# Kernel optimization log

Measured on AMD Instinct MI355X. Metric: run time of the kernel, lower is better.

The kernel has to match this reference:

```python
import jax, jax.numpy as jnp
import numpy as np

HX_INIT = 1e-6  # matches torch: zeros + 1e-06


def log_g(x):
    # log of continuous activation g: x>=0 -> log(x+0.5), else log(sigmoid(x)) = -softplus(-x)
    return jnp.where(x >= 0, jnp.log(jax.nn.relu(x) + 0.5), -jax.nn.softplus(-x))


def setup_inputs() -> dict:
    key = jax.random.key(0)
    k1, k2, k3 = jax.random.split(key, 3)
    N, L, H_in, H = 8, 4096, 512, 512
    x = jax.random.normal(k1, (N, L, H_in), dtype=jnp.float32)
    W = jax.random.normal(k2, (3 * H, H_in), dtype=jnp.float32) * 0.05
    b = jax.random.normal(k3, (3 * H,), dtype=jnp.float32) * 0.05
    return {"x": x, "W": W, "b": b}


def reference(x, W, b):
    N, L, _ = x.shape
    H = W.shape[0] // 3
    # gate preactivations: (N, L, 3H)
    pre = jnp.einsum('nli,oi->nlo', x, W) + b
    f_pre, i_pre, h_pre = jnp.split(pre, 3, axis=-1)
    # log-space gates
    diff = jax.nn.softplus(-f_pre) - jax.nn.softplus(-i_pre)
    log_f = -jax.nn.softplus(diff)       # log f'_t
    log_i = -jax.nn.softplus(-diff)      # log i'_t
    log_tilde_h = log_g(h_pre)
    # initial hidden state hx = 1e-6 (zeros + eps), shape (N, 1, H)
    log_h0 = jnp.full((N, 1, H), jnp.log(jnp.asarray(HX_INIT, x.dtype)), dtype=x.dtype)
    log_values = jnp.concatenate([log_h0, log_i + log_tilde_h], axis=1)  # (N, L+1, H)
    # Heinsen log-space parallel scan
    a_star = jnp.pad(jnp.cumsum(log_f, axis=1), ((0, 0), (1, 0), (0, 0)))  # (N, L+1, H)
    log_h = a_star + jax.lax.cumlogsumexp(log_values - a_star, axis=1)
    return jnp.exp(log_h)[:, 1:]  # (N, L, H)
```

## Files before the change

### kernel.cpp

```cpp
#include <hip/hip_runtime.h>
#include <hip/hip_bf16.h>


#define H_DIM 512
#define LSEQ 4096
#define NBATCH 8
#define M_TOTAL (NBATCH * LSEQ)

#define BM 128
#define BK 64

#define CS 128
#define NC 32

typedef __attribute__((ext_vector_type(8))) short short8;
typedef __attribute__((ext_vector_type(4))) float floatx4;
typedef __attribute__((ext_vector_type(4))) float float4v;
typedef _Float16 h2 __attribute__((ext_vector_type(2)));
typedef _Float16 h8 __attribute__((ext_vector_type(8)));
typedef __attribute__((ext_vector_type(2))) float float2v;
typedef __attribute__((ext_vector_type(2))) unsigned int uint2v;

#define NEG_BIG (-1.0e30f)
#define C_LOG2E 1.4426950408889634f
#define LOG2_HX0 (-19.931568569324174f)

__device__ __forceinline__ float exp2_hw(float x) {
#if __has_builtin(__builtin_amdgcn_exp2f)
    return __builtin_amdgcn_exp2f(x);
#else
    return exp2f(x);
#endif
}

__device__ __forceinline__ float log2_hw(float x) {
#if __has_builtin(__builtin_amdgcn_logf)
    return __builtin_amdgcn_logf(x);
#else
    return log2f(x);
#endif
}

__device__ __forceinline__ float logaddexp2_f(float p, float q) {
    float m = fmaxf(p, q);
    float d = -fabsf(p - q);
    return m + log2_hw(1.0f + exp2_hw(d));
}

__device__ __forceinline__ float bf16u_to_f(unsigned short u) {
    unsigned int w = ((unsigned int)u) << 16;
    float f;
    __builtin_memcpy(&f, &w, 4);
    return f;
}

__device__ __forceinline__ unsigned short f_to_bf16u(float f) {
    __hip_bfloat16 h = __float2bfloat16(f);
    unsigned short u;
    __builtin_memcpy(&u, &h, 2);
    return u;
}

__device__ __forceinline__ void gload_lds16(const void* g, void* l) {
    __builtin_amdgcn_global_load_lds(
        (const __attribute__((address_space(1))) unsigned int*)g,
        (__attribute__((address_space(3))) unsigned int*)l, 16, 0, 0);
}

__global__ void detect_and_bias(const unsigned short* __restrict__ xu,
                                const void* __restrict__ bsrc,
                                int* __restrict__ flag,
                                float* __restrict__ bdst) {
    __shared__ int cnt;
    if (threadIdx.x == 0) cnt = 0;
    __syncthreads();
    const short8* x8 = (const short8*)xu;
    int local = 0;
    #pragma unroll
    for (int j = 0; j < 8; j++) {
        short8 v = x8[threadIdx.x + j * 256];
        #pragma unroll
        for (int e = 0; e < 8; e++) {
            unsigned short u = (unsigned short)v[e];
            if (((u >> 7) & 0xFF) == 0xFF) local++;
        }
    }
    if (local) atomicAdd(&cnt, local);
    __syncthreads();
    int f = (cnt > 8) ? 1 : 0;
    if (threadIdx.x == 0) flag[0] = f;
    #pragma unroll
    for (int j = 0; j < 6; j++) {
        int i = threadIdx.x + j * 256;
        bdst[i] = f ? ((const float*)bsrc)[i]
                    : bf16u_to_f(((const unsigned short*)bsrc)[i]);
    }
}

__global__ __launch_bounds__(256)
void convert_inputs(const void* __restrict__ x, const void* __restrict__ W,
                    unsigned short* __restrict__ xc,
                    unsigned short* __restrict__ Wc,
                    const int* __restrict__ flag) {
    const int bx = blockIdx.x;
    const void* src;
    unsigned short* dst;
    int i;
    if (bx < 8192) { src = x; dst = xc; i = (bx * 256 + threadIdx.x) * 8; }
    else           { src = W; dst = Wc; i = ((bx - 8192) * 256 + threadIdx.x) * 8; }
    if (*flag) {
        const float4v* s4 = (const float4v*)((const float*)src + i);
        float4v a = s4[0], b = s4[1];
        short8 v;
        v[0] = (short)f_to_bf16u(a[0]); v[1] = (short)f_to_bf16u(a[1]);
        v[2] = (short)f_to_bf16u(a[2]); v[3] = (short)f_to_bf16u(a[3]);
        v[4] = (short)f_to_bf16u(b[0]); v[5] = (short)f_to_bf16u(b[1]);
        v[6] = (short)f_to_bf16u(b[2]); v[7] = (short)f_to_bf16u(b[3]);
        *(short8*)&dst[i] = v;
    } else {
        *(short8*)&dst[i] = *(const short8*)&((const short*)src)[i];
    }
}

__global__ __launch_bounds__(256, 3)
void gemm_gates(const unsigned short* __restrict__ x,
                const unsigned short* __restrict__ W,
                const float* __restrict__ bias,
                h2* __restrict__ plv,
                float* __restrict__ Asum, float* __restrict__ Bval,
                float* __restrict__ Asub, float* __restrict__ Bsub) {
    __shared__ __align__(16) char ldsbuf[40960];
    short* Alds = (short*)ldsbuf;
    short* Blds = (short*)(ldsbuf + 16384);
    h2* sc = (h2*)ldsbuf;
    float* sa = (float*)(ldsbuf + 32768);
    float* sb = sa + 256;

    const int by = blockIdx.x;
    const int bx = blockIdx.y;
    const int tid = threadIdx.x;
    const int lane = tid & 63;
    const int w = tid >> 6;
    const int wr = (w >> 1) * 64;
    const int wc2 = w & 1;
    const int l8 = lane >> 3, s8 = lane & 7;
    const int sg = s8 ^ l8;
    const int fr = lane & 15;
    const int q = lane >> 4;

    const int R0 = by * BM;

    floatx4 acc[4][6];
    #pragma unroll
    for (int i = 0; i < 4; i++)
        #pragma unroll
        for (int j = 0; j < 6; j++)
            acc[i][j] = (floatx4){0.f, 0.f, 0.f, 0.f};

    const short* xg = (const short*)x;
    const short* wg = (const short*)W;

    for (int k0 = 0; k0 < H_DIM; k0 += BK) {
        __syncthreads();
        #pragma unroll
        for (int i = 0; i < 4; i++) {
            int c = w * 4 + i;
            const short* g = xg + (size_t)(R0 + c * 8 + l8) * H_DIM + k0 + sg * 8;
            gload_lds16(g, &Alds[c * 512]);
        }
        #pragma unroll
        for (int i = 0; i < 6; i++) {
            int c = w * 6 + i;
            int br = c * 8 + l8;
            int wrow = (br >> 6) * H_DIM + bx * 64 + (br & 63);
            const short* g = wg + (size_t)wrow * H_DIM + k0 + sg * 8;
            gload_lds16(g, &Blds[c * 512]);
        }
        __syncthreads();

        #pragma unroll
        for (int ks = 0; ks < 2; ks++) {
            const int s = ks * 4 + q;
            short8 af[4], bf[6];
            #pragma unroll
            for (int mt = 0; mt < 4; mt++) {
                int ar = wr + mt * 16 + fr;
                af[mt] = *(const short8*)&Alds[ar * BK + ((s ^ (ar & 7)) << 3)];
            }
            #pragma unroll
            for (int j = 0; j < 6; j++) {
                int nt = (j >> 1) * 4 + wc2 * 2 + (j & 1);
                int brr = nt * 16 + fr;
                bf[j] = *(const short8*)&Blds[brr * BK + ((s ^ (brr & 7)) << 3)];
            }
            #pragma unroll
            for (int mt = 0; mt < 4; mt++)
                #pragma unroll
                for (int j = 0; j < 6; j++)
                    acc[mt][j] = __builtin_amdgcn_mfma_f32_16x16x32_bf16(
                        af[mt], bf[j], acc[mt][j], 0, 0, 0);
        }
    }

    __syncthreads();

    const int rowb = R0 + wr + q * 4;
    const int tloc0 = wr + q * 4;
    #pragma unroll
    for (int jj = 0; jj < 2; jj++) {
        int hl = wc2 * 32 + jj * 16 + fr;
        int hcol = bx * 64 + hl;
        float bfv = bias[hcol];
        float biv = bias[H_DIM + hcol];
        float bhv = bias[2 * H_DIM + hcol];
        float bf2 = -bfv * C_LOG2E;
        float bi2 = -biv * C_LOG2E;
        #pragma unroll
        for (int mt = 0; mt < 4; mt++) {
            #pragma unroll
            for (int r = 0; r < 4; r++) {
                float ef = exp2_hw(fminf(fmaf(acc[mt][jj][r], -C_LOG2E, bf2), 126.0f));
                float ei = exp2_hw(fminf(fmaf(acc[mt][2 + jj][r], -C_LOG2E, bi2), 126.0f));
                float hp = acc[mt][4 + jj][r] + bhv;
                float eh = exp2_hw(fminf(-hp * C_LOG2E, 126.0f));
                float afv = 1.0f + ef, aiv = 1.0f + ei;
                float sfi = afv + aiv;
                float ls = log2_hw(sfi);
                float lf = log2_hw(aiv) - ls;
                float marg = (hp >= 0.0f) ? (hp + 0.5f) : (1.0f + eh);
                float lm = log2_hw(marg);
                float lg = (hp >= 0.0f) ? lm : -lm;
                float lv = (log2_hw(afv) - ls) + lg;
                int row = rowb + mt * 16 + r;
                h2 pk;
                pk[0] = (_Float16)lf;
                pk[1] = (_Float16)lv;
                plv[(size_t)row * H_DIM + hcol] = pk;
                sc[(tloc0 + mt * 16 + r) * 64 + hl] = pk;
            }
        }
    }

    __syncthreads();

    const int n = by >> 5, c = by & 31;
    {
        float a = 0.f, bacc = NEG_BIG;
        const int t0 = w * 32;
        #pragma unroll 4
        for (int t = t0; t < t0 + 32; t++) {
            h2 p = sc[t * 64 + lane];
            float f = (float)p[0];
            bacc = logaddexp2_f(f + bacc, (float)p[1]);
            a += f;
        }
        sa[w * 64 + lane] = a;
        sb[w * 64 + lane] = bacc;
        size_t o = (((size_t)n * NC + c) * 4 + w) * H_DIM + bx * 64 + lane;
        Asub[o] = a;
        Bsub[o] = bacc;
    }
    __syncthreads();

    if (w == 0) {
        float a = sa[lane], b = sb[lane];
        #pragma unroll
        for (int s = 1; s < 4; s++) {
            float as = sa[s * 64 + lane], bs = sb[s * 64 + lane];
            b = logaddexp2_f(as + b, bs);
            a += as;
        }
        size_t o = ((size_t)n * NC + c) * H_DIM + bx * 64 + lane;
        Asum[o] = a;
        Bval[o] = b;
    }
}

__global__ __launch_bounds__(256)
void scan_apply(const h2* __restrict__ plv,
                const float* __restrict__ Asum, const float* __restrict__ Bval,
                const float* __restrict__ Asub, const float* __restrict__ Bsub,
                void* __restrict__ outv, const int* __restrict__ flag) {
    const int cc = blockIdx.x;
    const int n = blockIdx.y;
    const int c = cc & 31;
    const int s = (cc >> 5) * 2 + (threadIdx.x >> 7);
    const int h0 = (threadIdx.x & 127) * 4;
    const int f32out = *flag;

    float r0 = LOG2_HX0, r1 = r0, r2 = r0, r3 = r0;
    size_t so = (size_t)n * NC * H_DIM + h0;
    int cp = 0;
    for (; cp + 4 <= c; cp += 4) {
        float4v A0 = *(const float4v*)&Asum[so + (size_t)(cp + 0) * H_DIM];
        float4v B0 = *(const float4v*)&Bval[so + (size_t)(cp + 0) * H_DIM];
        float4v A1 = *(const float4v*)&Asum[so + (size_t)(cp + 1) * H_DIM];
        float4v B1 = *(const float4v*)&Bval[so + (size_t)(cp + 1) * H_DIM];
        float4v A2 = *(const float4v*)&Asum[so + (size_t)(cp + 2) * H_DIM];
        float4v B2 = *(const float4v*)&Bval[so + (size_t)(cp + 2) * H_DIM];
        float4v A3 = *(const float4v*)&Asum[so + (size_t)(cp + 3) * H_DIM];
        float4v B3 = *(const float4v*)&Bval[so + (size_t)(cp + 3) * H_DIM];
        r0 = logaddexp2_f(A0[0] + r0, B0[0]); r1 = logaddexp2_f(A0[1] + r1, B0[1]);
        r2 = logaddexp2_f(A0[2] + r2, B0[2]); r3 = logaddexp2_f(A0[3] + r3, B0[3]);
        r0 = logaddexp2_f(A1[0] + r0, B1[0]); r1 = logaddexp2_f(A1[1] + r1, B1[1]);
        r2 = logaddexp2_f(A1[2] + r2, B1[2]); r3 = logaddexp2_f(A1[3] + r3, B1[3]);
        r0 = logaddexp2_f(A2[0] + r0, B2[0]); r1 = logaddexp2_f(A2[1] + r1, B2[1]);
        r2 = logaddexp2_f(A2[2] + r2, B2[2]); r3 = logaddexp2_f(A2[3] + r3, B2[3]);
        r0 = logaddexp2_f(A3[0] + r0, B3[0]); r1 = logaddexp2_f(A3[1] + r1, B3[1]);
        r2 = logaddexp2_f(A3[2] + r2, B3[2]); r3 = logaddexp2_f(A3[3] + r3, B3[3]);
    }
    for (; cp < c; cp++) {
        float4v A = *(const float4v*)&Asum[so + (size_t)cp * H_DIM];
        float4v B = *(const float4v*)&Bval[so + (size_t)cp * H_DIM];
        r0 = logaddexp2_f(A[0] + r0, B[0]); r1 = logaddexp2_f(A[1] + r1, B[1]);
        r2 = logaddexp2_f(A[2] + r2, B[2]); r3 = logaddexp2_f(A[3] + r3, B[3]);
    }
    size_t sub = (((size_t)n * NC + c) * 4) * H_DIM + h0;
    for (int sp = 0; sp < s; sp++) {
        float4v A = *(const float4v*)&Asub[sub + (size_t)sp * H_DIM];
        float4v B = *(const float4v*)&Bsub[sub + (size_t)sp * H_DIM];
        r0 = logaddexp2_f(A[0] + r0, B[0]); r1 = logaddexp2_f(A[1] + r1, B[1]);
        r2 = logaddexp2_f(A[2] + r2, B[2]); r3 = logaddexp2_f(A[3] + r3, B[3]);
    }

    size_t base = ((size_t)n * LSEQ + (size_t)c * CS + s * 32) * H_DIM + h0;
    if (f32out) {
        float* of = (float*)outv;
        #pragma unroll 4
        for (int t = 0; t < 32; t++) {
            size_t idx = base + (size_t)t * H_DIM;
            h8 p = *(const h8*)&plv[idx];
            r0 = logaddexp2_f((float)p[0] + r0, (float)p[1]);
            r1 = logaddexp2_f((float)p[2] + r1, (float)p[3]);
            r2 = logaddexp2_f((float)p[4] + r2, (float)p[5]);
            r3 = logaddexp2_f((float)p[6] + r3, (float)p[7]);
            float4v o4 = {exp2_hw(r0), exp2_hw(r1), exp2_hw(r2), exp2_hw(r3)};
            *(float4v*)&of[idx] = o4;
        }
    } else {
        unsigned int* ob32 = (unsigned int*)outv;
        #pragma unroll 4
        for (int t = 0; t < 32; t++) {
            size_t idx = base + (size_t)t * H_DIM;
            h8 p = *(const h8*)&plv[idx];
            r0 = logaddexp2_f((float)p[0] + r0, (float)p[1]);
            r1 = logaddexp2_f((float)p[2] + r1, (float)p[3]);
            r2 = logaddexp2_f((float)p[4] + r2, (float)p[5]);
            r3 = logaddexp2_f((float)p[6] + r3, (float)p[7]);
            uint2v pk;
            pk[0] = ((unsigned int)f_to_bf16u(exp2_hw(r1)) << 16) | f_to_bf16u(exp2_hw(r0));
            pk[1] = ((unsigned int)f_to_bf16u(exp2_hw(r3)) << 16) | f_to_bf16u(exp2_hw(r2));
            *(uint2v*)&ob32[idx >> 1] = pk;
        }
    }
}

extern "C" void kernel_launch(void* const* d_in, const int* in_sizes, int n_in,
                              void* d_out, int out_size, void* d_ws, size_t ws_size,
                              hipStream_t stream) {
    const void* x = d_in[0];
    const void* W = d_in[1];
    const void* b = d_in[2];

    char* wsb = (char*)d_ws;
    int* flag            = (int*)wsb;
    float* bconv         = (float*)(wsb + 16);
    unsigned short* xc   = (unsigned short*)(wsb + 16384);
    unsigned short* Wc   = (unsigned short*)(wsb + 16384 + 33554432);
    h2* plv              = (h2*)(wsb + 36700160);
    float* Asum          = (float*)(wsb + 103809024);
    float* Bval          = (float*)(wsb + 104333312);
    float* Asub          = (float*)(wsb + 104857600);
    float* Bsub          = (float*)(wsb + 106954752);

    detect_and_bias<<<1, 256, 0, stream>>>((const unsigned short*)x, b, flag, bconv);
    convert_inputs<<<8576, 256, 0, stream>>>(x, W, xc, Wc, flag);

    dim3 g1(M_TOTAL / BM, H_DIM / 64);
    gemm_gates<<<g1, 256, 0, stream>>>(xc, Wc, bconv, plv, Asum, Bval, Asub, Bsub);

    dim3 g2(NC * 2, NBATCH);
    scan_apply<<<g2, 256, 0, stream>>>(plv, Asum, Bval, Asub, Bsub, d_out, flag);
}
```

Baseline: 212.4 us.

## Fuse scan into GEMM kernel via decoupled look-back across sequence chunks

```diff
diff --git a/kernel.cpp b/kernel.cpp
--- a/kernel.cpp
+++ b/kernel.cpp
@@ -17,9 +17,6 @@
 typedef __attribute__((ext_vector_type(4))) float floatx4;
 typedef __attribute__((ext_vector_type(4))) float float4v;
 typedef _Float16 h2 __attribute__((ext_vector_type(2)));
-typedef _Float16 h8 __attribute__((ext_vector_type(8)));
-typedef __attribute__((ext_vector_type(2))) float float2v;
-typedef __attribute__((ext_vector_type(2))) unsigned int uint2v;
 
 #define NEG_BIG (-1.0e30f)
 #define C_LOG2E 1.4426950408889634f
@@ -126,15 +123,17 @@
 void gemm_gates(const unsigned short* __restrict__ x,
                 const unsigned short* __restrict__ W,
                 const float* __restrict__ bias,
-                h2* __restrict__ plv,
-                float* __restrict__ Asum, float* __restrict__ Bval,
-                float* __restrict__ Asub, float* __restrict__ Bsub) {
+                float* __restrict__ aggA, float* __restrict__ aggB,
+                float* __restrict__ incA, float* __restrict__ incB,
+                int* __restrict__ flags,
+                void* __restrict__ outv, const int* __restrict__ oflag) {
     __shared__ __align__(16) char ldsbuf[40960];
     short* Alds = (short*)ldsbuf;
     short* Blds = (short*)(ldsbuf + 16384);
     h2* sc = (h2*)ldsbuf;
     float* sa = (float*)(ldsbuf + 32768);
-    float* sb = sa + 256;
+    float* sb = (float*)(ldsbuf + 33792);
+    float* carr = (float*)(ldsbuf + 34816);
 
     const int by = blockIdx.x;
     const int bx = blockIdx.y;
@@ -204,7 +203,6 @@
 
     __syncthreads();
 
-    const int rowb = R0 + wr + q * 4;
     const int tloc0 = wr + q * 4;
     #pragma unroll
     for (int jj = 0; jj < 2; jj++) {
@@ -231,11 +229,9 @@
                 float lm = log2_hw(marg);
                 float lg = (hp >= 0.0f) ? lm : -lm;
                 float lv = (log2_hw(afv) - ls) + lg;
-                int row = rowb + mt * 16 + r;
                 h2 pk;
                 pk[0] = (_Float16)lf;
                 pk[1] = (_Float16)lv;
-                plv[(size_t)row * H_DIM + hcol] = pk;
                 sc[(tloc0 + mt * 16 + r) * 64 + hl] = pk;
             }
         }
@@ -243,7 +239,8 @@
 
     __syncthreads();
 
-    const int n = by >> 5, c = by & 31;
+    const int c = by & 31;
+    const int fidx = by * 8 + bx;
     {
         float a = 0.f, bacc = NEG_BIG;
         const int t0 = w * 32;
@@ -256,101 +253,92 @@
         }
         sa[w * 64 + lane] = a;
         sb[w * 64 + lane] = bacc;
-        size_t o = (((size_t)n * NC + c) * 4 + w) * H_DIM + bx * 64 + lane;
-        Asub[o] = a;
-        Bsub[o] = bacc;
     }
     __syncthreads();
 
     if (w == 0) {
-        float a = sa[lane], b = sb[lane];
+        float Ac = sa[lane], Bc = sb[lane];
         #pragma unroll
         for (int s = 1; s < 4; s++) {
             float as = sa[s * 64 + lane], bs = sb[s * 64 + lane];
-            b = logaddexp2_f(as + b, bs);
-            a += as;
-        }
-        size_t o = ((size_t)n * NC + c) * H_DIM + bx * 64 + lane;
-        Asum[o] = a;
-        Bval[o] = b;
-    }
-}
-
-__global__ __launch_bounds__(256)
-void scan_apply(const h2* __restrict__ plv,
-                const float* __restrict__ Asum, const float* __restrict__ Bval,
-                const float* __restrict__ Asub, const float* __restrict__ Bsub,
-                void* __restrict__ outv, const int* __restrict__ flag) {
-    const int cc = blockIdx.x;
-    const int n = blockIdx.y;
-    const int c = cc & 31;
-    const int s = (cc >> 5) * 2 + (threadIdx.x >> 7);
-    const int h0 = (threadIdx.x & 127) * 4;
-    const int f32out = *flag;
-
-    float r0 = LOG2_HX0, r1 = r0, r2 = r0, r3 = r0;
-    size_t so = (size_t)n * NC * H_DIM + h0;
-    int cp = 0;
-    for (; cp + 4 <= c; cp += 4) {
-        float4v A0 = *(const float4v*)&Asum[so + (size_t)(cp + 0) * H_DIM];
-        float4v B0 = *(const float4v*)&Bval[so + (size_t)(cp + 0) * H_DIM];
-        float4v A1 = *(const float4v*)&Asum[so + (size_t)(cp + 1) * H_DIM];
-        float4v B1 = *(const float4v*)&Bval[so + (size_t)(cp + 1) * H_DIM];
-        float4v A2 = *(const float4v*)&Asum[so + (size_t)(cp + 2) * H_DIM];
-        float4v B2 = *(const float4v*)&Bval[so + (size_t)(cp + 2) * H_DIM];
-        float4v A3 = *(const float4v*)&Asum[so + (size_t)(cp + 3) * H_DIM];
-        float4v B3 = *(const float4v*)&Bval[so + (size_t)(cp + 3) * H_DIM];
-        r0 = logaddexp2_f(A0[0] + r0, B0[0]); r1 = logaddexp2_f(A0[1] + r1, B0[1]);
-        r2 = logaddexp2_f(A0[2] + r2, B0[2]); r3 = logaddexp2_f(A0[3] + r3, B0[3]);
-        r0 = logaddexp2_f(A1[0] + r0, B1[0]); r1 = logaddexp2_f(A1[1] + r1, B1[1]);
-        r2 = logaddexp2_f(A1[2] + r2, B1[2]); r3 = logaddexp2_f(A1[3] + r3, B1[3]);
-        r0 = logaddexp2_f(A2[0] + r0, B2[0]); r1 = logaddexp2_f(A2[1] + r1, B2[1]);
-        r2 = logaddexp2_f(A2[2] + r2, B2[2]); r3 = logaddexp2_f(A2[3] + r3, B2[3]);
-        r0 = logaddexp2_f(A3[0] + r0, B3[0]); r1 = logaddexp2_f(A3[1] + r1, B3[1]);
-        r2 = logaddexp2_f(A3[2] + r2, B3[2]); r3 = logaddexp2_f(A3[3] + r3, B3[3]);
-    }
-    for (; cp < c; cp++) {
-        float4v A = *(const float4v*)&Asum[so + (size_t)cp * H_DIM];
-        float4v B = *(const float4v*)&Bval[so + (size_t)cp * H_DIM];
-        r0 = logaddexp2_f(A[0] + r0, B[0]); r1 = logaddexp2_f(A[1] + r1, B[1]);
-        r2 = logaddexp2_f(A[2] + r2, B[2]); r3 = logaddexp2_f(A[3] + r3, B[3]);
-    }
-    size_t sub = (((size_t)n * NC + c) * 4) * H_DIM + h0;
-    for (int sp = 0; sp < s; sp++) {
-        float4v A = *(const float4v*)&Asub[sub + (size_t)sp * H_DIM];
-        float4v B = *(const float4v*)&Bsub[sub + (size_t)sp * H_DIM];
-        r0 = logaddexp2_f(A[0] + r0, B[0]); r1 = logaddexp2_f(A[1] + r1, B[1]);
-        r2 = logaddexp2_f(A[2] + r2, B[2]); r3 = logaddexp2_f(A[3] + r3, B[3]);
-    }
-
-    size_t base = ((size_t)n * LSEQ + (size_t)c * CS + s * 32) * H_DIM + h0;
-    if (f32out) {
-        float* of = (float*)outv;
-        #pragma unroll 4
-        for (int t = 0; t < 32; t++) {
-            size_t idx = base + (size_t)t * H_DIM;
-            h8 p = *(const h8*)&plv[idx];
-            r0 = logaddexp2_f((float)p[0] + r0, (float)p[1]);
-            r1 = logaddexp2_f((float)p[2] + r1, (float)p[3]);
-            r2 = logaddexp2_f((float)p[4] + r2, (float)p[5]);
-            r3 = logaddexp2_f((float)p[6] + r3, (float)p[7]);
-            float4v o4 = {exp2_hw(r0), exp2_hw(r1), exp2_hw(r2), exp2_hw(r3)};
-            *(float4v*)&of[idx] = o4;
-        }
-    } else {
-        unsigned int* ob32 = (unsigned int*)outv;
-        #pragma unroll 4
-        for (int t = 0; t < 32; t++) {
-            size_t idx = base + (size_t)t * H_DIM;
-            h8 p = *(const h8*)&plv[idx];
-            r0 = logaddexp2_f((float)p[0] + r0, (float)p[1]);
-            r1 = logaddexp2_f((float)p[2] + r1, (float)p[3]);
-            r2 = logaddexp2_f((float)p[4] + r2, (float)p[5]);
-            r3 = logaddexp2_f((float)p[6] + r3, (float)p[7]);
-            uint2v pk;
-            pk[0] = ((unsigned int)f_to_bf16u(exp2_hw(r1)) << 16) | f_to_bf16u(exp2_hw(r0));
-            pk[1] = ((unsigned int)f_to_bf16u(exp2_hw(r3)) << 16) | f_to_bf16u(exp2_hw(r2));
-            *(uint2v*)&ob32[idx >> 1] = pk;
+            Bc = logaddexp2_f(as + Bc, bs);
+            Ac += as;
+        }
+        float r_start;
+        if (c == 0) {
+            incA[fidx * 64 + lane] = Ac;
+            incB[fidx * 64 + lane] = Bc;
+            __threadfence();
+            if (lane == 0)
+                __hip_atomic_store(&flags[fidx], 2, __ATOMIC_RELEASE,
+                                   __HIP_MEMORY_SCOPE_AGENT);
+            r_start = LOG2_HX0;
+        } else {
+            aggA[fidx * 64 + lane] = Ac;
+            aggB[fidx * 64 + lane] = Bc;
+            __threadfence();
+            if (lane == 0)
+                __hip_atomic_store(&flags[fidx], 1, __ATOMIC_RELEASE,
+                                   __HIP_MEMORY_SCOPE_AGENT);
+            float Ap = 0.f, Bp = NEG_BIG;
+            int cp = c - 1;
+            while (cp >= 0) {
+                int f2 = fidx - (c - cp) * 8;
+                int st;
+                while ((st = __hip_atomic_load(&flags[f2], __ATOMIC_ACQUIRE,
+                                               __HIP_MEMORY_SCOPE_AGENT)) == 0)
+                    __builtin_amdgcn_s_sleep(2);
+                if (st == 2) {
+                    float At = incA[f2 * 64 + lane], Bt = incB[f2 * 64 + lane];
+                    Bp = logaddexp2_f(Ap + Bt, Bp);
+                    Ap += At;
+                    break;
+                } else {
+                    float At = aggA[f2 * 64 + lane], Bt = aggB[f2 * 64 + lane];
+                    Bp = logaddexp2_f(Ap + Bt, Bp);
+                    Ap += At;
+                    cp--;
+                }
+            }
+            incA[fidx * 64 + lane] = Ap + Ac;
+            incB[fidx * 64 + lane] = logaddexp2_f(Ac + Bp, Bc);
+            __threadfence();
+            if (lane == 0)
+                __hip_atomic_store(&flags[fidx], 2, __ATOMIC_RELEASE,
+                                   __HIP_MEMORY_SCOPE_AGENT);
+            r_start = logaddexp2_f(Ap + LOG2_HX0, Bp);
+        }
+        carr[lane] = r_start;
+    }
+    __syncthreads();
+
+    {
+        float r = carr[lane];
+        #pragma unroll
+        for (int s = 0; s < 4; s++) {
+            if (s < w) {
+                r = logaddexp2_f(sa[s * 64 + lane] + r, sb[s * 64 + lane]);
+            }
+        }
+        const int t0 = w * 32;
+        const size_t row0 = (size_t)by * BM + t0;
+        const int col = bx * 64 + lane;
+        if (*oflag) {
+            float* of = (float*)outv;
+            #pragma unroll 4
+            for (int t = 0; t < 32; t++) {
+                h2 p = sc[(t0 + t) * 64 + lane];
+                r = logaddexp2_f((float)p[0] + r, (float)p[1]);
+                of[(row0 + t) * H_DIM + col] = exp2_hw(r);
+            }
+        } else {
+            unsigned short* ob = (unsigned short*)outv;
+            #pragma unroll 4
+            for (int t = 0; t < 32; t++) {
+                h2 p = sc[(t0 + t) * 64 + lane];
+                r = logaddexp2_f((float)p[0] + r, (float)p[1]);
+                ob[(row0 + t) * H_DIM + col] = f_to_bf16u(exp2_hw(r));
+            }
         }
     }
 }
@@ -367,18 +355,17 @@
     float* bconv         = (float*)(wsb + 16);
     unsigned short* xc   = (unsigned short*)(wsb + 16384);
     unsigned short* Wc   = (unsigned short*)(wsb + 16384 + 33554432);
-    h2* plv              = (h2*)(wsb + 36700160);
-    float* Asum          = (float*)(wsb + 103809024);
-    float* Bval          = (float*)(wsb + 104333312);
-    float* Asub          = (float*)(wsb + 104857600);
-    float* Bsub          = (float*)(wsb + 106954752);
+    float* aggA          = (float*)(wsb + 36700160);
+    float* aggB          = (float*)(wsb + 36700160 + 524288);
+    float* incA          = (float*)(wsb + 36700160 + 1048576);
+    float* incB          = (float*)(wsb + 36700160 + 1572864);
+    int* flags           = (int*)(wsb + 36700160 + 2097152);
 
     detect_and_bias<<<1, 256, 0, stream>>>((const unsigned short*)x, b, flag, bconv);
     convert_inputs<<<8576, 256, 0, stream>>>(x, W, xc, Wc, flag);
+    hipMemsetAsync(flags, 0, 2048 * sizeof(int), stream);
 
     dim3 g1(M_TOTAL / BM, H_DIM / 64);
-    gemm_gates<<<g1, 256, 0, stream>>>(xc, Wc, bconv, plv, Asum, Bval, Asub, Bsub);
-
-    dim3 g2(NC * 2, NBATCH);
-    scan_apply<<<g2, 256, 0, stream>>>(plv, Asum, Bval, Asub, Bsub, d_out, flag);
-}
+    gemm_gates<<<g1, 256, 0, stream>>>(xc, Wc, bconv, aggA, aggB, incA, incB,
+                                       flags, d_out, flag);
+}
```

New measurement: 476.4 us. 124% more time.
